# Kernel optimization log

Measured on AMD Instinct MI355X. Metric: run time of the kernel, lower is better.

The kernel has to match this reference:

```python
import jax, jax.numpy as jnp
import numpy as np

B = 128  # batch


def _genperm(key, n):
    k1, k2 = jax.random.split(key)
    perm = jax.random.permutation(k1, n).astype(jnp.int32)
    scale = jax.random.uniform(k2, (n,), jnp.float32, 0.5, 2.0)
    return perm, scale


def _enc(x, p, s):  # y = A x with A[i, p[i]] = s[i]  (generalized permutation)
    return s * x[..., p]


def _dec(y, p, s):  # x = A^{-1} y
    return (y / s)[..., jnp.argsort(p)]


def _kconv(y, pin, sin, pout, sout, w, b, chw, stride):
    C, H, W = chw
    x = _dec(y, pin, sin)[:, :-1].reshape(-1, C, H, W)  # drop homogeneous 1
    pad = (w.shape[-1] - 1) // 2
    out = jax.lax.conv_general_dilated(x, w, (stride, stride), [(pad, pad), (pad, pad)],
                                       dimension_numbers=('NCHW', 'OIHW', 'NCHW'))
    out = out + b[None, :, None, None]
    flat = out.reshape(out.shape[0], -1)
    flat = jnp.concatenate([flat, jnp.ones((flat.shape[0], 1), flat.dtype)], axis=1)
    return _enc(flat, pout, sout)


def _krelu(y, pa, sa, pb, sb):  # B * relu(A^{-1} y); relu(1)=1 preserves homogeneous elt
    return _enc(jax.nn.relu(_dec(y, pa, sa)), pb, sb)


def _klin(y, pin, sin, pout, sout, W, b):
    x = _dec(y, pin, sin)[:, :-1]
    out = x @ W.T + b
    out = jnp.concatenate([out, jnp.ones((out.shape[0], 1), out.dtype)], axis=1)
    return _enc(out, pout, sout)


def setup_inputs():
    key = jax.random.key(0)
    ks = iter(jax.random.split(key, 64))
    d = {}
    N = {'0': 3 * 32 * 32 + 1, '1': 96 * 32 * 32 + 1, '3': 96 * 16 * 16 + 1,
         '4': 192 * 16 * 16 + 1, '6': 192 * 8 * 8 + 1, '9': 10 * 8 * 8 + 1,
         '10': 101, '11': 11}
    for name, n in [('0', N['0']), ('1a', N['1']), ('1b', N['1']), ('3a', N['3']),
                    ('3b', N['3']), ('4a', N['4']), ('4b', N['4']), ('6a', N['6']),
                    ('6b', N['6']), ('9a', N['9']), ('9b', N['9']), ('10a', N['10']),
                    ('10b', N['10']), ('11', N['11'])]:
        p, s = _genperm(next(ks), n)
        d['p' + name] = p
        d['s' + name] = s
    convs = [('1', (96, 3, 3, 3)), ('2', (96, 96, 3, 3)), ('3', (96, 96, 3, 3)),
             ('4', (192, 96, 3, 3)), ('5', (192, 192, 3, 3)), ('6', (192, 192, 3, 3)),
             ('7', (192, 192, 3, 3)), ('8', (192, 192, 1, 1)), ('9', (10, 192, 1, 1))]
    for name, shp in convs:
        fan_in = float(np.prod(shp[1:]))
        d['w' + name] = jax.random.normal(next(ks), shp, jnp.float32) / np.sqrt(fan_in)
        d['b' + name] = 0.01 * jax.random.normal(next(ks), (shp[0],), jnp.float32)
    d['fw1'] = jax.random.normal(next(ks), (100, 640), jnp.float32) / np.sqrt(640.0)
    d['fb1'] = 0.01 * jax.random.normal(next(ks), (100,), jnp.float32)
    d['fw2'] = jax.random.normal(next(ks), (10, 100), jnp.float32) / np.sqrt(100.0)
    d['fb2'] = 0.01 * jax.random.normal(next(ks), (10,), jnp.float32)
    x0 = jax.random.normal(next(ks), (B, 3 * 32 * 32), jnp.float32)
    x0h = jnp.concatenate([x0, jnp.ones((B, 1), jnp.float32)], axis=1)
    d['A0x0_affine'] = _enc(x0h, d['p0'], d['s0'])
    return d


def reference(A0x0_affine, w1, b1, w2, b2, w3, b3, w4, b4, w5, b5, w6, b6, w7, b7,
              w8, b8, w9, b9, fw1, fb1, fw2, fb2,
              p0, s0, p1a, s1a, p1b, s1b, p3a, s3a, p3b, s3b, p4a, s4a, p4b, s4b,
              p6a, s6a, p6b, s6b, p9a, s9a, p9b, s9b, p10a, s10a, p10b, s10b, p11, s11):
    y = _kconv(A0x0_affine, p0, s0, p1a, s1a, w1, b1, (3, 32, 32), 1)
    y = _krelu(y, p1a, s1a, p1b, s1b)                     # relu1
    y = _kconv(y, p1b, s1b, p1a, s1a, w2, b2, (96, 32, 32), 1)
    y = _krelu(y, p1a, s1a, p1b, s1b)                     # relu1 (reused)
    y = _kconv(y, p1b, s1b, p3a, s3a, w3, b3, (96, 32, 32), 2)   # conv3 (bn fused)
    y = _krelu(y, p3a, s3a, p3b, s3b)                     # relu3
    y = _kconv(y, p3b, s3b, p4a, s4a, w4, b4, (96, 16, 16), 1)
    y = _krelu(y, p4a, s4a, p4b, s4b)                     # relu4
    y = _kconv(y, p4b, s4b, p4a, s4a, w5, b5, (192, 16, 16), 1)
    y = _krelu(y, p4a, s4a, p4b, s4b)                     # relu4 (reused)
    y = _kconv(y, p4b, s4b, p6a, s6a, w6, b6, (192, 16, 16), 2)  # conv6 (bn fused)
    y = _krelu(y, p6a, s6a, p6b, s6b)                     # relu6
    y = _kconv(y, p6b, s6b, p6a, s6a, w7, b7, (192, 8, 8), 1)
    y = _krelu(y, p6a, s6a, p6b, s6b)                     # relu6 (reused)
    y = _kconv(y, p6b, s6b, p6a, s6a, w8, b8, (192, 8, 8), 1)
    y = _krelu(y, p6a, s6a, p6b, s6b)                     # relu6 (reused)
    y = _kconv(y, p6b, s6b, p9a, s9a, w9, b9, (192, 8, 8), 1)
    y = _krelu(y, p9a, s9a, p9b, s9b)                     # relu9
    y = _klin(y, p9b, s9b, p10a, s10a, fw1, fb1)          # fc1
    y = _krelu(y, p10a, s10a, p10b, s10b)                 # relu10
    y = _klin(y, p10b, s10b, p11, s11, fw2, fb2)          # fc2
    return y  # keyed output, shape (B, 11)
```

## Files before the change

### kernel.cpp

```cpp
#include <hip/hip_runtime.h>
#include <hip/hip_bf16.h>

#define BATCH 128
#define CDIV(a, b) (((a) + (b) - 1) / (b))

typedef __attribute__((ext_vector_type(8))) short short8;
typedef __attribute__((ext_vector_type(4))) float f32x4;

template <int V> struct ic { static constexpr int value = V; };
template <int... I> struct iseq {};
template <int N, int... I> struct mkseq : mkseq<N - 1, N - 1, I...> {};
template <int... I> struct mkseq<0, I...> { using type = iseq<I...>; };
template <class F, int... I>
__device__ __forceinline__ void unroll_all(F&& f, iseq<I...>) { (f(ic<I>{}), ...); }

__device__ __forceinline__ void gload_lds16(const void* g, void* l) {
    __builtin_amdgcn_global_load_lds(
        (const __attribute__((address_space(1))) void*)g,
        (__attribute__((address_space(3))) void*)l, 16, 0, 0);
}

__global__ void fill0_f32(float* __restrict__ p, int n) {
    int i = blockIdx.x * blockDim.x + threadIdx.x;
    if (i < n) p[i] = 0.0f;
}

__global__ void decode_kernel(const float* __restrict__ y, const int* __restrict__ p,
                              const float* __restrict__ s, float* __restrict__ x) {
    const int n = 3073;
    int idx = blockIdx.x * blockDim.x + threadIdx.x;
    if (idx >= BATCH * n) return;
    int i = idx % n, b = idx / n;
    int pi = p[i];
    if (pi >= 3072) return;
    float v = y[(size_t)b * n + i] / s[i];
    int c = pi >> 10; int r = pi & 1023; int h = r >> 5; int w = r & 31;
    x[((size_t)(b * 34 + h + 1) * 34 + (w + 1)) * 4 + c] = v;
}

struct HaloDesc { __hip_bfloat16* p; int Hp, Wp, C; };
struct Halo4 { HaloDesc d[4]; int cum[5]; int n; };

__global__ void halo_zero_multi(Halo4 h) {
    int idx = blockIdx.x * 256 + threadIdx.x;
    if (idx >= h.cum[h.n]) return;
    int seg = 0;
    while (idx >= h.cum[seg + 1]) ++seg;
    int local = idx - h.cum[seg];
    HaloDesc d = h.d[seg];
    int perB = (2 * d.Wp + 2 * (d.Hp - 2)) * d.C / 8;
    int b = local / perB;
    int r = (local % perB) * 8;
    int WpC = d.Wp * d.C;
    long addr;
    if (r < WpC) {
        addr = (long)(b * d.Hp) * WpC + r;
    } else if (r < 2 * WpC) {
        addr = (long)(b * d.Hp + d.Hp - 1) * WpC + (r - WpC);
    } else {
        int r3 = r - 2 * WpC;
        int sideN = (d.Hp - 2) * d.C;
        int side = r3 / sideN;
        int r4 = r3 % sideN;
        int row = 1 + r4 / d.C, c = r4 % d.C;
        addr = ((long)(b * d.Hp + row) * d.Wp + (side ? d.Wp - 1 : 0)) * d.C + c;
    }
    *(uint4*)((char*)d.p + addr * 2) = uint4{0, 0, 0, 0};
}

struct WtSeg { const float* src; __hip_bfloat16* dst; int Cout, Cin, KK, CoutPad; };
struct Wt8 { WtSeg s[8]; int cum[9]; };

__global__ void wt_transform_multi(Wt8 w) {
    int idx = blockIdx.x * 256 + threadIdx.x;
    if (idx >= w.cum[8]) return;
    int seg = 0;
    while (idx >= w.cum[seg + 1]) ++seg;
    int local = idx - w.cum[seg];
    WtSeg sg = w.s[seg];
    int c2 = local % 32; int t = local / 32;
    int co = t % sg.CoutPad; int t2 = t / sg.CoutPad;
    int KS = sg.Cin / 32;
    int kk = t2 % KS; int pos = t2 / KS;
    int cin = kk * 32 + c2;
    float v = (co < sg.Cout) ? sg.src[((size_t)co * sg.Cin + cin) * sg.KK + pos] : 0.0f;
    sg.dst[local] = __float2bfloat16(v);
}

__global__ __launch_bounds__(256) void conv1_kernel(
    const float* __restrict__ in, const float* __restrict__ w,
    const float* __restrict__ bias, __hip_bfloat16* __restrict__ out) {
    __shared__ float ws[96 * 27];
    __shared__ float bs[96];
    for (int i = threadIdx.x; i < 96 * 27; i += 256) ws[i] = w[i];
    if (threadIdx.x < 96) bs[threadIdx.x] = bias[threadIdx.x];
    __syncthreads();
    int idx = blockIdx.x * 256 + threadIdx.x;
    int q = idx & 3; int pix = idx >> 2;
    int b = pix >> 10, r = pix & 1023, oh = r >> 5, ow = r & 31;
    const float* ib = in + ((size_t)(b * 34 + oh) * 34 + ow) * 4;
    float patch[9][3];
#pragma unroll
    for (int ph = 0; ph < 3; ++ph)
#pragma unroll
        for (int pw = 0; pw < 3; ++pw) {
            float4 v = *(const float4*)(ib + ((size_t)ph * 34 + pw) * 4);
            patch[ph * 3 + pw][0] = v.x; patch[ph * 3 + pw][1] = v.y; patch[ph * 3 + pw][2] = v.z;
        }
    const int c0 = q * 24;
    float acc[24];
#pragma unroll
    for (int j = 0; j < 24; ++j) acc[j] = bs[c0 + j];
    for (int j = 0; j < 24; ++j) {
        const float* wc = &ws[(c0 + j) * 27];
#pragma unroll
        for (int ci = 0; ci < 3; ++ci)
#pragma unroll
            for (int pos = 0; pos < 9; ++pos)
                acc[j] = fmaf(patch[pos][ci], wc[ci * 9 + pos], acc[j]);
    }
    __hip_bfloat16* ob = out + ((size_t)(b * 34 + oh + 1) * 34 + ow + 1) * 96 + c0;
#pragma unroll
    for (int g = 0; g < 3; ++g) {
        union { uint4 u; unsigned short s[8]; } pk;
#pragma unroll
        for (int e = 0; e < 8; ++e) {
            __hip_bfloat16 hv = __float2bfloat16(fmaxf(acc[g * 8 + e], 0.0f));
            pk.s[e] = *(unsigned short*)&hv;
        }
        *(uint4*)(ob + g * 8) = pk.u;
    }
}

template <int CIN, int COUT, int HIN, int WIN, int STRIDE, int R,
          int WN, int MT, int NTW, int LA, int THREADS, int MINW>
__global__ __launch_bounds__(THREADS, MINW) void conv_pipe(
    const __hip_bfloat16* __restrict__ in,
    const __hip_bfloat16* __restrict__ wt,
    const float* __restrict__ bias,
    __hip_bfloat16* __restrict__ out) {
    constexpr int HOUT = HIN / STRIDE, WOUT = WIN / STRIDE;
    constexpr int Hp = HIN + 2, Wp = WIN + 2;
    constexpr int Hpo = HOUT + 2, Wpo = WOUT + 2;
    constexpr int D = 2 * R + 1;
    constexpr int KS = CIN / 32;
    constexpr int NSTEP = D * D * KS;
    constexpr int WAVES = THREADS / 64;
    static_assert(WAVES == WN, "one wave row");
    constexpr int BM = MT * 16;
    constexpr int BN = WN * NTW * 16;
    static_assert(BN == COUT, "block covers full N");
    static_assert(BM % WOUT == 0, "whole output rows");
    constexpr int BMR = BM / WOUT;
    constexpr int SUPR = (BMR - 1) * STRIDE + D;
    constexpr int CINU = CIN / 8;
    constexpr int UPP = CINU + 1;
    constexpr int ROWU = Wp * CINU;
    constexpr int TOTU = SUPR * ROWU;
    constexpr int DEPTH = LA + 1;

    __shared__ short8 ldsA[SUPR * Wp * UPP];
    __shared__ short8 ldsB[WAVES * DEPTH * NTW * 64];

    int wid = threadIdx.x >> 6;
    int lane = threadIdx.x & 63;
    int col = lane & 15, kgrp = lane >> 4;
    int n0 = wid * (NTW * 16);
    int sig_l = lane ^ ((lane >> 3) & 7);
    int su = col * 4 + kgrp; su ^= ((su >> 3) & 7);

    auto issueChunk = [&](int c, int slot) {
        const __hip_bfloat16* src = wt + ((size_t)c * COUT + n0) * 32 + sig_l * 8;
#pragma unroll
        for (int nt = 0; nt < NTW; ++nt)
            gload_lds16(src + nt * (16 * 32),
                        &ldsB[((wid * DEPTH + slot) * NTW + nt) * 64]);
    };

#pragma unroll
    for (int c = 0; c < LA; ++c)
        if (c < NSTEP) issueChunk(c, c);

    int m0 = blockIdx.x * BM;
    int gor = m0 / WOUT;
    int b = gor / HOUT;
    int oh0 = gor % HOUT;
    int r0 = oh0 * STRIDE + (1 - R);
    const __hip_bfloat16* gsrc = in + ((size_t)(b * Hp + r0) * Wp) * CIN;
    for (int g = threadIdx.x; g < TOTU; g += THREADS) {
        int row = g / ROWU;
        int ur = g - row * ROWU;
        int pix = ur / CINU;
        int c = ur - pix * CINU;
        ldsA[(row * Wp + pix) * UPP + c] = *reinterpret_cast<const short8*>(gsrc + (size_t)g * 8);
    }
    __syncthreads();

    int abaseu[MT];
#pragma unroll
    for (int mt = 0; mt < MT; ++mt) {
        int mloc = mt * 16 + col;
        int orow = mloc / WOUT, ocol = mloc % WOUT;
        abaseu[mt] = ((orow * STRIDE) * Wp + ocol * STRIDE + (1 - R)) * UPP + kgrp;
    }

    short8 af[2][MT], bf[2][NTW];
    f32x4 acc[MT][NTW] = {};

    auto readFrags = [&](int s, auto rIC) {
        constexpr int r = decltype(rIC)::value;
        int pos = s / KS, kk = s - (s / KS) * KS;
        int poff = ((pos / D) * Wp + (pos % D)) * UPP;
#pragma unroll
        for (int mt = 0; mt < MT; ++mt)
            af[r][mt] = ldsA[abaseu[mt] + poff + kk * 4];
        int slot = s % DEPTH;
#pragma unroll
        for (int nt = 0; nt < NTW; ++nt)
            bf[r][nt] = ldsB[((wid * DEPTH + slot) * NTW + nt) * 64 + su];
    };

    readFrags(0, ic<0>{});

    unroll_all([&](auto sc) {
        constexpr int s = decltype(sc)::value;
        if constexpr (s + LA < NSTEP) issueChunk(s + LA, (s + LA) % DEPTH);
        if constexpr (s + 1 < NSTEP) {
            constexpr int issuedMax = (s + LA < NSTEP - 1) ? (s + LA) : (NSTEP - 1);
            constexpr int NW = (issuedMax - (s + 1)) * NTW;
            asm volatile("s_waitcnt vmcnt(%0)" :: "i"(NW) : "memory");
            readFrags(s + 1, ic<(s + 1) & 1>{});
        }
#pragma unroll
        for (int nt = 0; nt < NTW; ++nt)
#pragma unroll
            for (int mt = 0; mt < MT; ++mt)
                acc[mt][nt] = __builtin_amdgcn_mfma_f32_16x16x32_bf16(
                    af[s & 1][mt], bf[s & 1][nt], acc[mt][nt], 0, 0, 0);
    }, typename mkseq<NSTEP>::type{});

#pragma unroll
    for (int mt = 0; mt < MT; ++mt) {
#pragma unroll
        for (int nt = 0; nt < NTW; ++nt) {
            int cout = n0 + nt * 16 + col;
            float bv = bias[cout];
#pragma unroll
            for (int rg = 0; rg < 4; ++rg) {
                int mloc = mt * 16 + kgrp * 4 + rg;
                int orow = mloc / WOUT, ocol = mloc % WOUT;
                float v = fmaxf(acc[mt][nt][rg] + bv, 0.0f);
                out[((size_t)(b * Hpo + oh0 + orow + 1) * Wpo + ocol + 1) * COUT + cout] =
                    __float2bfloat16(v);
            }
        }
    }
}

template <int CIN, int COUT, int HIN, int WIN, int STRIDE, int R,
          int WM, int WN, int MT, int NTW, int PW, int THREADS, int MINW>
__global__ __launch_bounds__(THREADS, MINW) void conv_lds(
    const __hip_bfloat16* __restrict__ in,
    const __hip_bfloat16* __restrict__ wt,
    const float* __restrict__ bias,
    __hip_bfloat16* __restrict__ out) {
    constexpr int HOUT = HIN / STRIDE, WOUT = WIN / STRIDE;
    constexpr int Hp = HIN + 2, Wp = WIN + 2;
    constexpr int Hpo = HOUT + 2, Wpo = WOUT + 2;
    constexpr int D = 2 * R + 1;
    constexpr int KS = CIN / 32;
    constexpr int NSTEP = D * D * KS;
    constexpr int BM = WM * MT * 16;
    constexpr int BN = WN * NTW * 16;
    static_assert(BN == COUT, "block covers full N");
    static_assert(BM % WOUT == 0, "block tile = whole output rows");
    static_assert(THREADS / 64 == WM * WN, "wave count");
    constexpr int BMR = BM / WOUT;
    constexpr int SUPR = (BMR - 1) * STRIDE + D;
    constexpr int CINU = CIN / 8;
    constexpr int UPP = CINU + 1;
    constexpr int ROWU = Wp * CINU;
    constexpr int TOTU = SUPR * ROWU;

    __shared__ short8 lds[SUPR * Wp * UPP];

    int m0 = blockIdx.x * BM;
    int gor = m0 / WOUT;
    int b = gor / HOUT;
    int oh0 = gor % HOUT;
    int r0 = oh0 * STRIDE + (1 - R);

    const __hip_bfloat16* gsrc = in + ((size_t)(b * Hp + r0) * Wp) * CIN;
    for (int g = threadIdx.x; g < TOTU; g += THREADS) {
        int row = g / ROWU;
        int ur = g - row * ROWU;
        int pix = ur / CINU;
        int c = ur - pix * CINU;
        lds[(row * Wp + pix) * UPP + c] = *reinterpret_cast<const short8*>(gsrc + (size_t)g * 8);
    }
    __syncthreads();

    int wid = threadIdx.x >> 6;
    int lane = threadIdx.x & 63;
    int col = lane & 15, kgrp = lane >> 4;
    int wm = wid / WN, wn = wid % WN;
    int n0 = wn * NTW * 16;

    int apix[MT];
#pragma unroll
    for (int mt = 0; mt < MT; ++mt) {
        int mloc = (wm * MT + mt) * 16 + col;
        int orow = mloc / WOUT, ocol = mloc % WOUT;
        apix[mt] = (orow * STRIDE) * Wp + ocol * STRIDE + (1 - R);
    }
    const __hip_bfloat16* bbase[NTW];
#pragma unroll
    for (int nt = 0; nt < NTW; ++nt)
        bbase[nt] = wt + (size_t)(n0 + nt * 16 + col) * 32 + kgrp * 8;

    short8 abuf[3][MT];
    short8 bbuf[PW][NTW];
    f32x4 acc[MT][NTW] = {};

    auto ldA = [&](int s, int slot) {
        int pos = s / KS, kk = s - (s / KS) * KS;
        int dh = pos / D, dw = pos - dh * D;
        int poff = dh * Wp + dw;
#pragma unroll
        for (int mt = 0; mt < MT; ++mt)
            abuf[slot][mt] = lds[(apix[mt] + poff) * UPP + kk * 4 + kgrp];
    };
    auto ldB = [&](int s, int slot) {
        size_t off = (size_t)s * (COUT * 32);
#pragma unroll
        for (int nt = 0; nt < NTW; ++nt)
            bbuf[slot][nt] = *reinterpret_cast<const short8*>(bbase[nt] + off);
    };

#pragma unroll
    for (int s = 0; s < PW - 1; ++s)
        if (s < NSTEP) ldB(s, s);
    ldA(0, 0);
    if (1 < NSTEP) ldA(1, 1);
    __builtin_amdgcn_sched_barrier(0);

#pragma unroll
    for (int s = 0; s < NSTEP; ++s) {
        if (s + PW - 1 < NSTEP) ldB(s + PW - 1, (s + PW - 1) % PW);
        if (s + 2 < NSTEP) ldA(s + 2, (s + 2) % 3);
        __builtin_amdgcn_sched_barrier(0);
#pragma unroll
        for (int nt = 0; nt < NTW; ++nt)
#pragma unroll
            for (int mt = 0; mt < MT; ++mt)
                acc[mt][nt] = __builtin_amdgcn_mfma_f32_16x16x32_bf16(
                    abuf[s % 3][mt], bbuf[s % PW][nt], acc[mt][nt], 0, 0, 0);
    }

#pragma unroll
    for (int mt = 0; mt < MT; ++mt) {
#pragma unroll
        for (int nt = 0; nt < NTW; ++nt) {
            int cout = n0 + nt * 16 + col;
            float bv = bias[cout];
#pragma unroll
            for (int rg = 0; rg < 4; ++rg) {
                int mloc = (wm * MT + mt) * 16 + kgrp * 4 + rg;
                int orow = mloc / WOUT, ocol = mloc % WOUT;
                float v = fmaxf(acc[mt][nt][rg] + bv, 0.0f);
                out[((size_t)(b * Hpo + oh0 + orow + 1) * Wpo + ocol + 1) * COUT + cout] =
                    __float2bfloat16(v);
            }
        }
    }
}

__global__ __launch_bounds__(256) void conv9_kernel(
    const __hip_bfloat16* __restrict__ in, const __hip_bfloat16* __restrict__ wt,
    const float* __restrict__ bias, float* __restrict__ out) {
    int wid = threadIdx.x >> 6;
    int lane = threadIdx.x & 63;
    int wave = blockIdx.x * 4 + wid;
    int m0 = wave * 16;
    int col = lane & 15;
    int kgrp = lane >> 4;
    int m = m0 + col;
    int b = m >> 6; int r = m & 63; int oh = r >> 3; int ow = r & 7;
    const __hip_bfloat16* abase = in + ((size_t)(b * 10 + oh + 1) * 10 + ow + 1) * 192 + kgrp * 8;
    f32x4 acc = {};
#pragma unroll
    for (int kk = 0; kk < 6; ++kk) {
        short8 bfr = *reinterpret_cast<const short8*>(wt + ((size_t)kk * 16 + col) * 32 + kgrp * 8);
        short8 a = *reinterpret_cast<const short8*>(abase + kk * 32);
        acc = __builtin_amdgcn_mfma_f32_16x16x32_bf16(a, bfr, acc, 0, 0, 0);
    }
    if (col < 10) {
        float bv = bias[col];
#pragma unroll
        for (int rg = 0; rg < 4; ++rg) {
            int m2 = m0 + kgrp * 4 + rg;
            int b2 = m2 >> 6; int r2 = m2 & 63;
            out[(size_t)b2 * 640 + col * 64 + r2] = fmaxf(acc[rg] + bv, 0.0f);
        }
    }
}

__global__ __launch_bounds__(128) void head_kernel(
    const float* __restrict__ act9, const float* __restrict__ fw1, const float* __restrict__ fb1,
    const float* __restrict__ fw2, const float* __restrict__ fb2,
    const int* __restrict__ p11, const float* __restrict__ s11, float* __restrict__ out) {
    __shared__ float x[640];
    __shared__ float h[100];
    __shared__ float o[10];
    int b = blockIdx.x, t = threadIdx.x;
    for (int i = t; i < 160; i += 128)
        ((float4*)x)[i] = ((const float4*)(act9 + (size_t)b * 640))[i];
    __syncthreads();
    if (t < 100) {
        float acc = fb1[t];
        const float4* wr = (const float4*)(fw1 + (size_t)t * 640);
        const float4* xv = (const float4*)x;
#pragma unroll 4
        for (int i = 0; i < 160; ++i) {
            float4 wv = wr[i], qv = xv[i];
            acc = fmaf(wv.x, qv.x, acc); acc = fmaf(wv.y, qv.y, acc);
            acc = fmaf(wv.z, qv.z, acc); acc = fmaf(wv.w, qv.w, acc);
        }
        h[t] = fmaxf(acc, 0.0f);
    }
    __syncthreads();
    if (t < 10) {
        float acc = fb2[t];
        for (int i = 0; i < 100; ++i) acc = fmaf(h[i], fw2[t * 100 + i], acc);
        o[t] = acc;
    }
    __syncthreads();
    if (t < 11) {
        int pi = p11[t];
        out[(size_t)b * 11 + t] = s11[t] * (pi == 10 ? 1.0f : o[pi]);
    }
}

extern "C" void kernel_launch(void* const* d_in, const int* in_sizes, int n_in,
                              void* d_out, int out_size, void* d_ws, size_t ws_size,
                              hipStream_t stream) {
    const int*   p0  = (const int*)  d_in[0];
    const float* s0  = (const float*)d_in[1];
    const int*   p11 = (const int*)  d_in[26];
    const float* s11 = (const float*)d_in[27];
    const float* w1 = (const float*)d_in[28]; const float* b1 = (const float*)d_in[29];
    const float* w2 = (const float*)d_in[30]; const float* b2 = (const float*)d_in[31];
    const float* w3 = (const float*)d_in[32]; const float* b3 = (const float*)d_in[33];
    const float* w4 = (const float*)d_in[34]; const float* b4 = (const float*)d_in[35];
    const float* w5 = (const float*)d_in[36]; const float* b5 = (const float*)d_in[37];
    const float* w6 = (const float*)d_in[38]; const float* b6 = (const float*)d_in[39];
    const float* w7 = (const float*)d_in[40]; const float* b7 = (const float*)d_in[41];
    const float* w8 = (const float*)d_in[42]; const float* b8 = (const float*)d_in[43];
    const float* w9 = (const float*)d_in[44]; const float* b9 = (const float*)d_in[45];
    const float* fw1 = (const float*)d_in[46]; const float* fb1 = (const float*)d_in[47];
    const float* fw2 = (const float*)d_in[48]; const float* fb2 = (const float*)d_in[49];
    const float* A0 = (const float*)d_in[50];
    float* out = (float*)d_out;

    size_t off = 0;
    auto alloc = [&](size_t bytes) {
        void* p = (char*)d_ws + off;
        off += (bytes + 255) & ~(size_t)255;
        return p;
    };
    const size_t SZ_3434_96  = (size_t)BATCH * 34 * 34 * 96 * 2;
    const size_t SZ_1818_96  = (size_t)BATCH * 18 * 18 * 96 * 2;
    const size_t SZ_1818_192 = (size_t)BATCH * 18 * 18 * 192 * 2;

    float* dec = (float*)alloc((size_t)BATCH * 34 * 34 * 4 * 4);
    __hip_bfloat16* regA = (__hip_bfloat16*)alloc(SZ_3434_96);
    __hip_bfloat16* regB = (__hip_bfloat16*)alloc(SZ_3434_96);
    __hip_bfloat16* regC = (__hip_bfloat16*)alloc(SZ_1818_96);
    __hip_bfloat16* regD = (__hip_bfloat16*)alloc(SZ_1818_192);
    __hip_bfloat16* wt2 = (__hip_bfloat16*)alloc((size_t)9 * 96 * 96 * 2);
    __hip_bfloat16* wt3 = (__hip_bfloat16*)alloc((size_t)9 * 96 * 96 * 2);
    __hip_bfloat16* wt4 = (__hip_bfloat16*)alloc((size_t)9 * 192 * 96 * 2);
    __hip_bfloat16* wt5 = (__hip_bfloat16*)alloc((size_t)9 * 192 * 192 * 2);
    __hip_bfloat16* wt6 = (__hip_bfloat16*)alloc((size_t)9 * 192 * 192 * 2);
    __hip_bfloat16* wt7 = (__hip_bfloat16*)alloc((size_t)9 * 192 * 192 * 2);
    __hip_bfloat16* wt8 = (__hip_bfloat16*)alloc((size_t)1 * 192 * 192 * 2);
    __hip_bfloat16* wt9 = (__hip_bfloat16*)alloc((size_t)16 * 192 * 2);
    float* act9 = (float*)alloc((size_t)BATCH * 640 * 4);

    const int TPB = 256;

    int decN = BATCH * 34 * 34 * 4;
    fill0_f32<<<CDIV(decN, TPB), TPB, 0, stream>>>(dec, decN);
    decode_kernel<<<CDIV(BATCH * 3073, TPB), TPB, 0, stream>>>(A0, p0, s0, dec);

    Wt8 wts;
    wts.s[0] = {w2, wt2, 96, 96, 9, 96};
    wts.s[1] = {w3, wt3, 96, 96, 9, 96};
    wts.s[2] = {w4, wt4, 192, 96, 9, 192};
    wts.s[3] = {w5, wt5, 192, 192, 9, 192};
    wts.s[4] = {w6, wt6, 192, 192, 9, 192};
    wts.s[5] = {w7, wt7, 192, 192, 9, 192};
    wts.s[6] = {w8, wt8, 192, 192, 1, 192};
    wts.s[7] = {w9, wt9, 10, 192, 1, 16};
    wts.cum[0] = 0;
    for (int i = 0; i < 8; ++i)
        wts.cum[i + 1] = wts.cum[i] + wts.s[i].KK * wts.s[i].CoutPad * wts.s[i].Cin;
    wt_transform_multi<<<CDIV(wts.cum[8], TPB), TPB, 0, stream>>>(wts);

    auto chunks = [](int Hp, int Wp, int C) { return BATCH * (2 * Wp + 2 * (Hp - 2)) * C / 8; };
    Halo4 h0;
    h0.d[0] = {regA, 34, 34, 96};
    h0.d[1] = {regB, 34, 34, 96};
    h0.d[2] = {regC, 18, 18, 96};
    h0.d[3] = {regD, 18, 18, 192};
    h0.n = 4; h0.cum[0] = 0;
    for (int i = 0; i < 4; ++i)
        h0.cum[i + 1] = h0.cum[i] + chunks(h0.d[i].Hp, h0.d[i].Wp, h0.d[i].C);
    halo_zero_multi<<<CDIV(h0.cum[4], TPB), TPB, 0, stream>>>(h0);

    conv1_kernel<<<2048, 256, 0, stream>>>(dec, w1, b1, regA);
    conv_pipe<96, 96, 32, 32, 1, 1, 2, 4, 3, 3, 128, 2><<<2048, 128, 0, stream>>>(regA, wt2, b2, regB);
    Halo4 h5; h5.d[0] = {regA, 18, 18, 192}; h5.n = 1;
    h5.cum[0] = 0; h5.cum[1] = chunks(18, 18, 192);
    halo_zero_multi<<<CDIV(h5.cum[1], TPB), TPB, 0, stream>>>(h5);
    conv_pipe<96, 96, 32, 32, 2, 1, 2, 2, 3, 3, 128, 2><<<1024, 128, 0, stream>>>(regB, wt3, b3, regC);
    conv_pipe<96, 192, 16, 16, 1, 1, 4, 4, 3, 3, 256, 2><<<512, 256, 0, stream>>>(regC, wt4, b4, regD);
    Halo4 h6; h6.d[0] = {regC, 10, 10, 192}; h6.n = 1;
    h6.cum[0] = 0; h6.cum[1] = chunks(10, 10, 192);
    halo_zero_multi<<<CDIV(h6.cum[1], TPB), TPB, 0, stream>>>(h6);
    conv_pipe<192, 192, 16, 16, 1, 1, 4, 4, 3, 4, 256, 1><<<512, 256, 0, stream>>>(regD, wt5, b5, regA);
    conv_pipe<192, 192, 16, 16, 2, 1, 4, 1, 3, 2, 256, 2><<<512, 256, 0, stream>>>(regA, wt6, b6, regC);
    conv_pipe<192, 192, 8, 8, 1, 1, 4, 2, 3, 3, 256, 2><<<256, 256, 0, stream>>>(regC, wt7, b7, regD);
    conv_lds<192, 192, 8, 8, 1, 0, 1, 4, 1, 3, 6, 256, 3><<<512, 256, 0, stream>>>(regD, wt8, b8, regB);
    conv9_kernel<<<128, 256, 0, stream>>>(regB, wt9, b9, act9);
    head_kernel<<<BATCH, 128, 0, stream>>>(act9, fw1, fb1, fw2, fb2, p11, s11, out);
}
```

Baseline: 210.9 us.

## Deepen conv_pipe fragment prefetch to two steps and decouple LDS ring depth

```diff
diff --git a/kernel.cpp b/kernel.cpp
--- a/kernel.cpp
+++ b/kernel.cpp
@@ -133,7 +133,7 @@
 }
 
 template <int CIN, int COUT, int HIN, int WIN, int STRIDE, int R,
-          int WN, int MT, int NTW, int LA, int THREADS, int MINW>
+          int WN, int MT, int NTW, int LA, int DEPTH, int THREADS, int MINW>
 __global__ __launch_bounds__(THREADS, MINW) void conv_pipe(
     const __hip_bfloat16* __restrict__ in,
     const __hip_bfloat16* __restrict__ wt,
@@ -151,13 +151,13 @@
     constexpr int BN = WN * NTW * 16;
     static_assert(BN == COUT, "block covers full N");
     static_assert(BM % WOUT == 0, "whole output rows");
+    static_assert(LA >= 3 && DEPTH >= 3 && DEPTH >= LA - 1, "pipeline depth");
     constexpr int BMR = BM / WOUT;
     constexpr int SUPR = (BMR - 1) * STRIDE + D;
     constexpr int CINU = CIN / 8;
     constexpr int UPP = CINU + 1;
     constexpr int ROWU = Wp * CINU;
     constexpr int TOTU = SUPR * ROWU;
-    constexpr int DEPTH = LA + 1;
 
     __shared__ short8 ldsA[SUPR * Wp * UPP];
     __shared__ short8 ldsB[WAVES * DEPTH * NTW * 64];
@@ -166,11 +166,10 @@
     int lane = threadIdx.x & 63;
     int col = lane & 15, kgrp = lane >> 4;
     int n0 = wid * (NTW * 16);
-    int sig_l = lane ^ ((lane >> 3) & 7);
-    int su = col * 4 + kgrp; su ^= ((su >> 3) & 7);
+    int su = col * 4 + kgrp;
 
     auto issueChunk = [&](int c, int slot) {
-        const __hip_bfloat16* src = wt + ((size_t)c * COUT + n0) * 32 + sig_l * 8;
+        const __hip_bfloat16* src = wt + ((size_t)c * COUT + n0) * 32 + lane * 8;
 #pragma unroll
         for (int nt = 0; nt < NTW; ++nt)
             gload_lds16(src + nt * (16 * 32),
@@ -179,7 +178,7 @@
 
 #pragma unroll
     for (int c = 0; c < LA; ++c)
-        if (c < NSTEP) issueChunk(c, c);
+        if (c < NSTEP) issueChunk(c, c % DEPTH);
 
     int m0 = blockIdx.x * BM;
     int gor = m0 / WOUT;
@@ -204,7 +203,7 @@
         abaseu[mt] = ((orow * STRIDE) * Wp + ocol * STRIDE + (1 - R)) * UPP + kgrp;
     }
 
-    short8 af[2][MT], bf[2][NTW];
+    short8 af[3][MT], bf[3][NTW];
     f32x4 acc[MT][NTW] = {};
 
     auto readFrags = [&](int s, auto rIC) {
@@ -221,22 +220,24 @@
     };
 
     readFrags(0, ic<0>{});
+    if (1 < NSTEP) readFrags(1, ic<1>{});
 
     unroll_all([&](auto sc) {
         constexpr int s = decltype(sc)::value;
         if constexpr (s + LA < NSTEP) issueChunk(s + LA, (s + LA) % DEPTH);
-        if constexpr (s + 1 < NSTEP) {
-            constexpr int issuedMax = (s + LA < NSTEP - 1) ? (s + LA) : (NSTEP - 1);
-            constexpr int NW = (issuedMax - (s + 1)) * NTW;
+        if constexpr (s + 2 < NSTEP) {
+            constexpr int I = (s + LA < NSTEP - 1) ? (s + LA) : (NSTEP - 1);
+            constexpr int NW0 = (I - (s + 2)) * NTW;
+            constexpr int NW = NW0 < 0 ? 0 : NW0;
             asm volatile("s_waitcnt vmcnt(%0)" :: "i"(NW) : "memory");
-            readFrags(s + 1, ic<(s + 1) & 1>{});
+            readFrags(s + 2, ic<(s + 2) % 3>{});
         }
 #pragma unroll
         for (int nt = 0; nt < NTW; ++nt)
 #pragma unroll
             for (int mt = 0; mt < MT; ++mt)
                 acc[mt][nt] = __builtin_amdgcn_mfma_f32_16x16x32_bf16(
-                    af[s & 1][mt], bf[s & 1][nt], acc[mt][nt], 0, 0, 0);
+                    af[s % 3][mt], bf[s % 3][nt], acc[mt][nt], 0, 0, 0);
     }, typename mkseq<NSTEP>::type{});
 
 #pragma unroll
@@ -519,18 +520,18 @@
     halo_zero_multi<<<CDIV(h0.cum[4], TPB), TPB, 0, stream>>>(h0);
 
     conv1_kernel<<<2048, 256, 0, stream>>>(dec, w1, b1, regA);
-    conv_pipe<96, 96, 32, 32, 1, 1, 2, 4, 3, 3, 128, 2><<<2048, 128, 0, stream>>>(regA, wt2, b2, regB);
+    conv_pipe<96, 96, 32, 32, 1, 1, 2, 4, 3, 4, 4, 128, 2><<<2048, 128, 0, stream>>>(regA, wt2, b2, regB);
     Halo4 h5; h5.d[0] = {regA, 18, 18, 192}; h5.n = 1;
     h5.cum[0] = 0; h5.cum[1] = chunks(18, 18, 192);
     halo_zero_multi<<<CDIV(h5.cum[1], TPB), TPB, 0, stream>>>(h5);
-    conv_pipe<96, 96, 32, 32, 2, 1, 2, 2, 3, 3, 128, 2><<<1024, 128, 0, stream>>>(regB, wt3, b3, regC);
-    conv_pipe<96, 192, 16, 16, 1, 1, 4, 4, 3, 3, 256, 2><<<512, 256, 0, stream>>>(regC, wt4, b4, regD);
+    conv_pipe<96, 96, 32, 32, 2, 1, 2, 2, 3, 4, 4, 128, 2><<<1024, 128, 0, stream>>>(regB, wt3, b3, regC);
+    conv_pipe<96, 192, 16, 16, 1, 1, 4, 4, 3, 4, 4, 256, 2><<<512, 256, 0, stream>>>(regC, wt4, b4, regD);
     Halo4 h6; h6.d[0] = {regC, 10, 10, 192}; h6.n = 1;
     h6.cum[0] = 0; h6.cum[1] = chunks(10, 10, 192);
     halo_zero_multi<<<CDIV(h6.cum[1], TPB), TPB, 0, stream>>>(h6);
-    conv_pipe<192, 192, 16, 16, 1, 1, 4, 4, 3, 4, 256, 1><<<512, 256, 0, stream>>>(regD, wt5, b5, regA);
-    conv_pipe<192, 192, 16, 16, 2, 1, 4, 1, 3, 2, 256, 2><<<512, 256, 0, stream>>>(regA, wt6, b6, regC);
-    conv_pipe<192, 192, 8, 8, 1, 1, 4, 2, 3, 3, 256, 2><<<256, 256, 0, stream>>>(regC, wt7, b7, regD);
+    conv_pipe<192, 192, 16, 16, 1, 1, 4, 4, 3, 3, 3, 256, 2><<<512, 256, 0, stream>>>(regD, wt5, b5, regA);
+    conv_pipe<192, 192, 16, 16, 2, 1, 4, 1, 3, 3, 3, 256, 2><<<512, 256, 0, stream>>>(regA, wt6, b6, regC);
+    conv_pipe<192, 192, 8, 8, 1, 1, 4, 2, 3, 4, 4, 256, 2><<<256, 256, 0, stream>>>(regC, wt7, b7, regD);
     conv_lds<192, 192, 8, 8, 1, 0, 1, 4, 1, 3, 6, 256, 3><<<512, 256, 0, stream>>>(regD, wt8, b8, regB);
     conv9_kernel<<<128, 256, 0, stream>>>(regB, wt9, b9, act9);
     head_kernel<<<BATCH, 128, 0, stream>>>(act9, fw1, fb1, fw2, fb2, p11, s11, out);
```

Result: no change. 207.2 us (-1.7%).
